# Kernel tuning notes

Hardware: AMD Instinct MI355X
Metric: run time of the kernel (lower is better)

The kernel has to match this reference:

```python
import jax, jax.numpy as jnp
import numpy as np

SQRT2 = 1.4142135623730951  # lrelu def_gain
LRELU_SLOPE = 0.2
EPS = 1e-8


def setup_inputs() -> dict:
    key = jax.random.key(0)
    k1, k2, k3, k4 = jax.random.split(key, 4)
    B, C_in, C_out, H, W, K, DLAT = 8, 512, 512, 32, 32, 3, 512
    x = jax.random.normal(k1, (B, C_in, H, W), dtype=jnp.float32)
    y = jax.random.normal(k2, (B, DLAT), dtype=jnp.float32)
    # init_std = 1.0 since use_wscale=True, lrmul=1
    weight = jax.random.normal(k3, (C_out, C_in, K, K), dtype=jnp.float32)
    mod_weight = jax.random.normal(k4, (C_in, DLAT), dtype=jnp.float32)
    bias = jnp.ones((C_in,), dtype=jnp.float32)
    return {"x": x, "y": y, "weight": weight, "mod_weight": mod_weight, "bias": bias}


def reference(x, y, weight, mod_weight, bias):
    B, C_in, H, W = x.shape
    C_out, _, K, _ = weight.shape
    dlat = mod_weight.shape[1]
    w_mul_mod = dlat ** (-0.5)  # EqualizedLinear wscale; conv w_mul is unused in forward
    # style: s = sqrt(2) * lrelu(y @ W_mod^T + b)
    s = y @ (mod_weight * w_mul_mod).T  # [B, C_in]
    s = jax.nn.leaky_relu(s + bias, LRELU_SLOPE) * SQRT2
    # modulate per-sample weights: [B, C_out, C_in, K, K]
    ww = weight[None] * s[:, None, :, None, None]
    # demodulate
    d = jax.lax.rsqrt(jnp.sum(ww * ww, axis=(2, 3, 4)) + EPS)  # [B, C_out]
    ww = ww * d[:, :, None, None, None]
    # fused grouped conv: groups = batch
    xg = x.reshape(1, B * C_in, H, W)
    wg = ww.reshape(B * C_out, C_in, K, K)
    out = jax.lax.conv_general_dilated(
        xg, wg, window_strides=(1, 1), padding="SAME",
        dimension_numbers=("NCHW", "OIHW", "NCHW"),
        feature_group_count=B)
    return out.reshape(B, C_out, H, W)
```

## Files before the change

kernel.cpp:

```cpp
#include <hip/hip_runtime.h>
#include <hip/hip_bf16.h>

typedef float f32x4 __attribute__((ext_vector_type(4)));
typedef short bf16x8 __attribute__((ext_vector_type(8)));

#define LRELU_SLOPE 0.2f
#define SQRT2F 1.4142135623730951f
#define MODSCALE 0.044194173824159216f

#define GLL(SRC, DST)                                                       \
  __builtin_amdgcn_global_load_lds(                                         \
      (const __attribute__((address_space(1))) unsigned int*)(SRC),         \
      (__attribute__((address_space(3))) unsigned int*)(DST), 16, 0, 0)

__global__ __launch_bounds__(64) void style_kernel(const float* __restrict__ y,
                                                   const float* __restrict__ mw,
                                                   const float* __restrict__ bias,
                                                   float* __restrict__ s) {
  int ci = blockIdx.x;
  int l = threadIdx.x;
  const float4* mwr = reinterpret_cast<const float4*>(mw + ci * 512);
  float4 m0 = mwr[2 * l], m1 = mwr[2 * l + 1];
  float acc[8];
#pragma unroll
  for (int b = 0; b < 8; ++b) {
    const float4* yr = reinterpret_cast<const float4*>(y + b * 512);
    float4 y0 = yr[2 * l], y1 = yr[2 * l + 1];
    acc[b] = m0.x * y0.x + m0.y * y0.y + m0.z * y0.z + m0.w * y0.w +
             m1.x * y1.x + m1.y * y1.y + m1.z * y1.z + m1.w * y1.w;
  }
#pragma unroll
  for (int off = 32; off > 0; off >>= 1) {
#pragma unroll
    for (int b = 0; b < 8; ++b) acc[b] += __shfl_xor(acc[b], off, 64);
  }
  if (l < 8) {
    float v = acc[l] * MODSCALE + bias[ci];
    v = v > 0.f ? v : LRELU_SLOPE * v;
    s[l * 512 + ci] = v * SQRT2F;
  }
}

__global__ __launch_bounds__(256) void wprep_kernel(const float* __restrict__ w,
                                                    __hip_bfloat16* __restrict__ wt,
                                                    float* __restrict__ wsq) {
  int idx = blockIdx.x * 256 + threadIdx.x;
  const float* p = w + (size_t)idx * 9;
  float v[9];
  float sq = 0.f;
#pragma unroll
  for (int t = 0; t < 9; ++t) {
    v[t] = p[t];
    sq += v[t] * v[t];
  }
  wsq[idx] = sq;
#pragma unroll
  for (int t = 0; t < 9; ++t) wt[t * 262144 + idx] = __float2bfloat16(v[t]);
}

__global__ __launch_bounds__(64) void demod_kernel(const float* __restrict__ wsq,
                                                   const float* __restrict__ s,
                                                   float* __restrict__ d) {
  int co = blockIdx.x;
  int l = threadIdx.x;
  const float4* qr = reinterpret_cast<const float4*>(wsq + co * 512);
  float4 q0 = qr[2 * l], q1 = qr[2 * l + 1];
  float acc[8];
#pragma unroll
  for (int b = 0; b < 8; ++b) {
    const float4* sr = reinterpret_cast<const float4*>(s + b * 512);
    float4 s0 = sr[2 * l], s1 = sr[2 * l + 1];
    acc[b] = q0.x * s0.x * s0.x + q0.y * s0.y * s0.y + q0.z * s0.z * s0.z +
             q0.w * s0.w * s0.w + q1.x * s1.x * s1.x + q1.y * s1.y * s1.y +
             q1.z * s1.z * s1.z + q1.w * s1.w * s1.w;
  }
#pragma unroll
  for (int off = 32; off > 0; off >>= 1) {
#pragma unroll
    for (int b = 0; b < 8; ++b) acc[b] += __shfl_xor(acc[b], off, 64);
  }
  if (l < 8) d[l * 512 + co] = rsqrtf(acc[l] + 1e-8f);
}

__global__ __launch_bounds__(256) void xs_kernel(const float* __restrict__ x,
                                                 const float* __restrict__ s,
                                                 __hip_bfloat16* __restrict__ xsp) {
  int bid = blockIdx.x;
  int cc = bid & 7;
  int h = (bid >> 3) & 31;
  int b = bid >> 8;
  int tid = threadIdx.x;
  __shared__ __hip_bfloat16 tile[32][72];

  int cil = tid >> 2;
  int w0 = (tid & 3) * 8;
  int ci = cc * 64 + cil;
  const float* xp = x + (((size_t)(b * 512 + ci) * 32 + h) << 5) + w0;
  float sv = s[b * 512 + ci];
  float4 a0 = *reinterpret_cast<const float4*>(xp);
  float4 a1 = *reinterpret_cast<const float4*>(xp + 4);
  tile[w0 + 0][cil] = __float2bfloat16(a0.x * sv);
  tile[w0 + 1][cil] = __float2bfloat16(a0.y * sv);
  tile[w0 + 2][cil] = __float2bfloat16(a0.z * sv);
  tile[w0 + 3][cil] = __float2bfloat16(a0.w * sv);
  tile[w0 + 4][cil] = __float2bfloat16(a1.x * sv);
  tile[w0 + 5][cil] = __float2bfloat16(a1.y * sv);
  tile[w0 + 6][cil] = __float2bfloat16(a1.z * sv);
  tile[w0 + 7][cil] = __float2bfloat16(a1.w * sv);
  __syncthreads();

  int wloc = tid >> 3;
  int cj = (tid & 7) * 8;
  int4 v = *reinterpret_cast<const int4*>(&tile[wloc][cj]);
  unsigned off = (unsigned)((b * 34 + h + 1) * 34 + (wloc + 1)) * 512 + cc * 64 + cj;
  *reinterpret_cast<int4*>(xsp + off) = v;
}

__global__ __launch_bounds__(512, 2) void conv_kernel(const __hip_bfloat16* __restrict__ xsp,
                                                      const __hip_bfloat16* __restrict__ wt,
                                                      const float* __restrict__ dmod,
                                                      float* __restrict__ out) {
  __shared__ __hip_bfloat16 As_[2][224 * 64];
  __shared__ __hip_bfloat16 Bs_[2][3 * 128 * 64];
  const int bid = blockIdx.x;
  const int xcd = bid & 7, slot = bid >> 3;
  const int bm = xcd * 8 + (slot >> 2);
  const int bn = slot & 3;
  const int tid = threadIdx.x;
  const int wv = tid >> 6;
  const int l = tid & 63;
  const int kg = wv >> 2;
  const int wr = (wv >> 1) & 1, wc = wv & 1;
  const int bb = bm >> 3;
  const int h0 = (bm & 7) << 2;

  const int swz = (((l & 7) ^ (l >> 3)) << 3);
  unsigned boff[2];
#pragma unroll
  for (int j = 0; j < 2; ++j) {
    int row = ((j * 8 + wv) << 3) + (l >> 3);
    boff[j] = (unsigned)((bn << 7) + row) * 512 + swz;
  }
  unsigned ahoff[4];
  int adst[4];
#pragma unroll
  for (int j = 0; j < 4; ++j) {
    int rb = j < 3 ? j * 64 + wv * 8 : 192 + (wv & 3) * 8;
    int r = rb + (l >> 3);
    int rc = r > 203 ? 203 : r;
    int hr = rc / 34, hc = rc - hr * 34;
    ahoff[j] = (unsigned)((bb * 34 + h0 + hr) * 34 + hc) * 512 + (((l & 7) ^ (r & 7)) << 3);
    adst[j] = rb;
  }
  int pb[4];
#pragma unroll
  for (int m = 0; m < 4; ++m)
    pb[m] = ((wr << 1) + (m >> 1)) * 34 + ((m & 1) << 4) + (l & 15);

  f32x4 acc[4][4];
#pragma unroll
  for (int n = 0; n < 4; ++n)
#pragma unroll
    for (int m = 0; m < 4; ++m) acc[n][m] = (f32x4)0.f;

  auto stageB = [&](__hip_bfloat16* Bn, int t, int k0c) {
    const __hip_bfloat16* src = wt + t * 262144 + k0c * 64;
#pragma unroll
    for (int j = 0; j < 2; ++j)
      GLL(src + boff[j], Bn + ((j * 8 + wv) << 9));
  };
  auto stageA1 = [&](__hip_bfloat16* An, int j, int kn) {
    GLL(xsp + ahoff[j] + kn * 64, An + (adst[j] << 6));
  };
  auto phase = [&](const __hip_bfloat16* Aq, const __hip_bfloat16* Bq, int dh, int dw) {
    const int cb = (kg << 2) + (l >> 4);
    bf16x8 af[4], bfr[4];
#pragma unroll
    for (int m = 0; m < 4; ++m) {
      int p = pb[m] + dh * 34 + dw;
      af[m] = *reinterpret_cast<const bf16x8*>(Aq + p * 64 + ((cb ^ (p & 7)) << 3));
    }
#pragma unroll
    for (int n = 0; n < 4; ++n) {
      int row = (wc << 6) + (n << 4) + (l & 15);
      bfr[n] = *reinterpret_cast<const bf16x8*>(Bq + row * 64 + ((cb ^ (l & 7)) << 3));
    }
    __builtin_amdgcn_s_setprio(1);
#pragma unroll
    for (int n = 0; n < 4; ++n)
#pragma unroll
      for (int m = 0; m < 4; ++m)
        acc[n][m] = __builtin_amdgcn_mfma_f32_16x16x32_bf16(bfr[n], af[m], acc[n][m], 0, 0, 0);
    __builtin_amdgcn_s_setprio(0);
  };

#define SB0 __builtin_amdgcn_sched_barrier(0)
#define WAITBAR0                                            \
  asm volatile("s_waitcnt vmcnt(0)" ::: "memory");          \
  __builtin_amdgcn_s_barrier();                             \
  SB0

#pragma unroll
  for (int j = 0; j < 4; ++j) stageA1(&As_[0][0], j, 0);
  SB0;
  stageB(&Bs_[0][0] + 0 * 8192, 0, 0);
  stageB(&Bs_[0][0] + 1 * 8192, 1, 0);
  stageB(&Bs_[0][0] + 2 * 8192, 2, 0);

#pragma unroll 1
  for (int k0 = 0; k0 < 8; ++k0) {
    const __hip_bfloat16* Aq = &As_[k0 & 1][0];
    __hip_bfloat16* An = &As_[(k0 + 1) & 1][0];
    __hip_bfloat16* Br = &Bs_[k0 & 1][0];
    __hip_bfloat16* Bo = &Bs_[(k0 & 1) ^ 1][0];
    const int kn = k0 + 1;
    WAITBAR0;
    stageB(Bo + 0 * 8192, 3, k0);
    stageB(Bo + 1 * 8192, 4, k0);
    stageB(Bo + 2 * 8192, 5, k0);
    if (k0 < 7) { stageA1(An, 0, kn); stageA1(An, 1, kn); }
    SB0;
    phase(Aq, Br + 0 * 8192, 0, 0);
    phase(Aq, Br + 1 * 8192, 0, 1);
    phase(Aq, Br + 2 * 8192, 0, 2);
    WAITBAR0;
    stageB(Br + 0 * 8192, 6, k0);
    stageB(Br + 1 * 8192, 7, k0);
    stageB(Br + 2 * 8192, 8, k0);
    if (k0 < 7) { stageA1(An, 2, kn); stageA1(An, 3, kn); }
    SB0;
    phase(Aq, Bo + 0 * 8192, 1, 0);
    phase(Aq, Bo + 1 * 8192, 1, 1);
    phase(Aq, Bo + 2 * 8192, 1, 2);
    WAITBAR0;
    if (k0 < 7) {
      stageB(Bo + 0 * 8192, 0, kn);
      stageB(Bo + 1 * 8192, 1, kn);
      stageB(Bo + 2 * 8192, 2, kn);
    }
    SB0;
    phase(Aq, Br + 0 * 8192, 2, 0);
    phase(Aq, Br + 1 * 8192, 2, 1);
    phase(Aq, Br + 2 * 8192, 2, 2);
  }
#undef WAITBAR0
#undef SB0

  float* red = reinterpret_cast<float*>(&Bs_[0][0]);
  __syncthreads();
  if (kg == 1) {
#pragma unroll
    for (int n = 0; n < 4; ++n)
#pragma unroll
      for (int m = 0; m < 4; ++m)
        *reinterpret_cast<f32x4*>(red + (n * 4 + m) * 1024 + (wv & 3) * 256 + l * 4) =
            acc[n][m];
  }
  __syncthreads();
  if (kg == 0) {
    const int pixbase = ((bm & 7) << 7) + (wr << 6) + (l & 15);
    const int cob = (bn << 7) + (wc << 6) + ((l >> 4) << 2);
    float* ob = out + ((size_t)bb << 19);
    const float* drow = dmod + bb * 512;
#pragma unroll
    for (int n = 0; n < 4; ++n) {
#pragma unroll
      for (int m = 0; m < 4; ++m)
        acc[n][m] += *reinterpret_cast<const f32x4*>(red + (n * 4 + m) * 1024 + wv * 256 + l * 4);
#pragma unroll
      for (int jj = 0; jj < 4; ++jj) {
        const int co = cob + (n << 4) + jj;
        const float dv = drow[co];
        float* orow = ob + ((unsigned)co << 10) + pixbase;
#pragma unroll
        for (int m = 0; m < 4; ++m) orow[m << 4] = acc[n][m][jj] * dv;
      }
    }
  }
}

extern "C" void kernel_launch(void* const* d_in, const int* in_sizes, int n_in,
                              void* d_out, int out_size, void* d_ws, size_t ws_size,
                              hipStream_t stream) {
  (void)in_sizes; (void)n_in; (void)out_size; (void)ws_size;
  const float* x = (const float*)d_in[0];
  const float* y = (const float*)d_in[1];
  const float* w = (const float*)d_in[2];
  const float* mw = (const float*)d_in[3];
  const float* bias = (const float*)d_in[4];
  float* out = (float*)d_out;

  char* ws = (char*)d_ws;
  float* s = (float*)(ws + 0);
  float* dmod = (float*)(ws + 16384);
  float* wsq = (float*)(ws + 32768);
  __hip_bfloat16* wt = (__hip_bfloat16*)(ws + 1081344);
  __hip_bfloat16* xsp = (__hip_bfloat16*)(ws + 5799936);

  hipMemsetAsync(xsp, 0, 9469952, stream);
  style_kernel<<<512, 64, 0, stream>>>(y, mw, bias, s);
  wprep_kernel<<<1024, 256, 0, stream>>>(w, wt, wsq);
  demod_kernel<<<512, 64, 0, stream>>>(wsq, s, dmod);
  xs_kernel<<<2048, 256, 0, stream>>>(x, s, xsp);
  conv_kernel<<<256, 512, 0, stream>>>(xsp, wt, dmod, out);
}
```

Baseline: 70.22 us.

## Fuse prep kernels, zero only halo, and deepen conv weight pipeline to four slots

```diff
diff --git a/kernel.cpp b/kernel.cpp
--- a/kernel.cpp
+++ b/kernel.cpp
@@ -13,107 +13,123 @@
       (const __attribute__((address_space(1))) unsigned int*)(SRC),         \
       (__attribute__((address_space(3))) unsigned int*)(DST), 16, 0, 0)
 
-__global__ __launch_bounds__(64) void style_kernel(const float* __restrict__ y,
+__global__ __launch_bounds__(256) void prep_kernel(const float* __restrict__ w,
+                                                   const float* __restrict__ y,
                                                    const float* __restrict__ mw,
                                                    const float* __restrict__ bias,
-                                                   float* __restrict__ s) {
-  int ci = blockIdx.x;
-  int l = threadIdx.x;
-  const float4* mwr = reinterpret_cast<const float4*>(mw + ci * 512);
-  float4 m0 = mwr[2 * l], m1 = mwr[2 * l + 1];
-  float acc[8];
-#pragma unroll
-  for (int b = 0; b < 8; ++b) {
-    const float4* yr = reinterpret_cast<const float4*>(y + b * 512);
-    float4 y0 = yr[2 * l], y1 = yr[2 * l + 1];
-    acc[b] = m0.x * y0.x + m0.y * y0.y + m0.z * y0.z + m0.w * y0.w +
-             m1.x * y1.x + m1.y * y1.y + m1.z * y1.z + m1.w * y1.w;
-  }
-#pragma unroll
-  for (int off = 32; off > 0; off >>= 1) {
-#pragma unroll
-    for (int b = 0; b < 8; ++b) acc[b] += __shfl_xor(acc[b], off, 64);
-  }
-  if (l < 8) {
-    float v = acc[l] * MODSCALE + bias[ci];
-    v = v > 0.f ? v : LRELU_SLOPE * v;
-    s[l * 512 + ci] = v * SQRT2F;
+                                                   __hip_bfloat16* __restrict__ wt,
+                                                   float* __restrict__ wsq,
+                                                   float* __restrict__ s,
+                                                   __hip_bfloat16* __restrict__ xsp) {
+  const int bid = blockIdx.x;
+  const int tid = threadIdx.x;
+  if (bid < 1024) {
+    int idx = bid * 256 + tid;
+    const float* p = w + (size_t)idx * 9;
+    float v[9];
+    float sq = 0.f;
+#pragma unroll
+    for (int t = 0; t < 9; ++t) {
+      v[t] = p[t];
+      sq += v[t] * v[t];
+    }
+    wsq[idx] = sq;
+#pragma unroll
+    for (int t = 0; t < 9; ++t) wt[t * 262144 + idx] = __float2bfloat16(v[t]);
+  } else if (bid < 1152) {
+    int l = tid & 63;
+    int ci = (bid - 1024) * 4 + (tid >> 6);
+    const float4* mwr = reinterpret_cast<const float4*>(mw + ci * 512);
+    float4 m0 = mwr[2 * l], m1 = mwr[2 * l + 1];
+    float acc[8];
+#pragma unroll
+    for (int b = 0; b < 8; ++b) {
+      const float4* yr = reinterpret_cast<const float4*>(y + b * 512);
+      float4 y0 = yr[2 * l], y1 = yr[2 * l + 1];
+      acc[b] = m0.x * y0.x + m0.y * y0.y + m0.z * y0.z + m0.w * y0.w +
+               m1.x * y1.x + m1.y * y1.y + m1.z * y1.z + m1.w * y1.w;
+    }
+#pragma unroll
+    for (int off = 32; off > 0; off >>= 1) {
+#pragma unroll
+      for (int b = 0; b < 8; ++b) acc[b] += __shfl_xor(acc[b], off, 64);
+    }
+    if (l < 8) {
+      float v = acc[l] * MODSCALE + bias[ci];
+      v = v > 0.f ? v : LRELU_SLOPE * v;
+      s[l * 512 + ci] = v * SQRT2F;
+    }
+  } else {
+    int i = (bid - 1152) * 256 + tid;
+    int b = i / 8448;
+    int r = i - b * 8448;
+    int pos = r >> 6;
+    int cj = (r & 63) << 3;
+    int hr, hc;
+    if (pos < 34) { hr = 0; hc = pos; }
+    else if (pos < 68) { hr = 33; hc = pos - 34; }
+    else if (pos < 100) { hr = pos - 67; hc = 0; }
+    else { hr = pos - 99; hc = 33; }
+    unsigned off = (unsigned)((b * 34 + hr) * 34 + hc) * 512 + cj;
+    int4 z = {0, 0, 0, 0};
+    *reinterpret_cast<int4*>(xsp + off) = z;
   }
 }
 
-__global__ __launch_bounds__(256) void wprep_kernel(const float* __restrict__ w,
-                                                    __hip_bfloat16* __restrict__ wt,
-                                                    float* __restrict__ wsq) {
-  int idx = blockIdx.x * 256 + threadIdx.x;
-  const float* p = w + (size_t)idx * 9;
-  float v[9];
-  float sq = 0.f;
-#pragma unroll
-  for (int t = 0; t < 9; ++t) {
-    v[t] = p[t];
-    sq += v[t] * v[t];
-  }
-  wsq[idx] = sq;
-#pragma unroll
-  for (int t = 0; t < 9; ++t) wt[t * 262144 + idx] = __float2bfloat16(v[t]);
-}
-
-__global__ __launch_bounds__(64) void demod_kernel(const float* __restrict__ wsq,
-                                                   const float* __restrict__ s,
-                                                   float* __restrict__ d) {
-  int co = blockIdx.x;
-  int l = threadIdx.x;
-  const float4* qr = reinterpret_cast<const float4*>(wsq + co * 512);
-  float4 q0 = qr[2 * l], q1 = qr[2 * l + 1];
-  float acc[8];
-#pragma unroll
-  for (int b = 0; b < 8; ++b) {
-    const float4* sr = reinterpret_cast<const float4*>(s + b * 512);
-    float4 s0 = sr[2 * l], s1 = sr[2 * l + 1];
-    acc[b] = q0.x * s0.x * s0.x + q0.y * s0.y * s0.y + q0.z * s0.z * s0.z +
-             q0.w * s0.w * s0.w + q1.x * s1.x * s1.x + q1.y * s1.y * s1.y +
-             q1.z * s1.z * s1.z + q1.w * s1.w * s1.w;
-  }
-#pragma unroll
-  for (int off = 32; off > 0; off >>= 1) {
-#pragma unroll
-    for (int b = 0; b < 8; ++b) acc[b] += __shfl_xor(acc[b], off, 64);
-  }
-  if (l < 8) d[l * 512 + co] = rsqrtf(acc[l] + 1e-8f);
-}
-
-__global__ __launch_bounds__(256) void xs_kernel(const float* __restrict__ x,
-                                                 const float* __restrict__ s,
-                                                 __hip_bfloat16* __restrict__ xsp) {
-  int bid = blockIdx.x;
-  int cc = bid & 7;
-  int h = (bid >> 3) & 31;
-  int b = bid >> 8;
-  int tid = threadIdx.x;
-  __shared__ __hip_bfloat16 tile[32][72];
-
-  int cil = tid >> 2;
-  int w0 = (tid & 3) * 8;
-  int ci = cc * 64 + cil;
-  const float* xp = x + (((size_t)(b * 512 + ci) * 32 + h) << 5) + w0;
-  float sv = s[b * 512 + ci];
-  float4 a0 = *reinterpret_cast<const float4*>(xp);
-  float4 a1 = *reinterpret_cast<const float4*>(xp + 4);
-  tile[w0 + 0][cil] = __float2bfloat16(a0.x * sv);
-  tile[w0 + 1][cil] = __float2bfloat16(a0.y * sv);
-  tile[w0 + 2][cil] = __float2bfloat16(a0.z * sv);
-  tile[w0 + 3][cil] = __float2bfloat16(a0.w * sv);
-  tile[w0 + 4][cil] = __float2bfloat16(a1.x * sv);
-  tile[w0 + 5][cil] = __float2bfloat16(a1.y * sv);
-  tile[w0 + 6][cil] = __float2bfloat16(a1.z * sv);
-  tile[w0 + 7][cil] = __float2bfloat16(a1.w * sv);
-  __syncthreads();
-
-  int wloc = tid >> 3;
-  int cj = (tid & 7) * 8;
-  int4 v = *reinterpret_cast<const int4*>(&tile[wloc][cj]);
-  unsigned off = (unsigned)((b * 34 + h + 1) * 34 + (wloc + 1)) * 512 + cc * 64 + cj;
-  *reinterpret_cast<int4*>(xsp + off) = v;
+__global__ __launch_bounds__(256) void xsdem_kernel(const float* __restrict__ x,
+                                                    const float* __restrict__ s,
+                                                    const float* __restrict__ wsq,
+                                                    __hip_bfloat16* __restrict__ xsp,
+                                                    float* __restrict__ d) {
+  const int bid = blockIdx.x;
+  const int tid = threadIdx.x;
+  if (bid < 2048) {
+    int cc = bid & 7;
+    int h = (bid >> 3) & 31;
+    int b = bid >> 8;
+    __shared__ __hip_bfloat16 tile[32][72];
+    int cil = tid >> 2;
+    int w0 = (tid & 3) * 8;
+    int ci = cc * 64 + cil;
+    const float* xp = x + (((size_t)(b * 512 + ci) * 32 + h) << 5) + w0;
+    float sv = s[b * 512 + ci];
+    float4 a0 = *reinterpret_cast<const float4*>(xp);
+    float4 a1 = *reinterpret_cast<const float4*>(xp + 4);
+    tile[w0 + 0][cil] = __float2bfloat16(a0.x * sv);
+    tile[w0 + 1][cil] = __float2bfloat16(a0.y * sv);
+    tile[w0 + 2][cil] = __float2bfloat16(a0.z * sv);
+    tile[w0 + 3][cil] = __float2bfloat16(a0.w * sv);
+    tile[w0 + 4][cil] = __float2bfloat16(a1.x * sv);
+    tile[w0 + 5][cil] = __float2bfloat16(a1.y * sv);
+    tile[w0 + 6][cil] = __float2bfloat16(a1.z * sv);
+    tile[w0 + 7][cil] = __float2bfloat16(a1.w * sv);
+    __syncthreads();
+    int wloc = tid >> 3;
+    int cj = (tid & 7) * 8;
+    int4 v = *reinterpret_cast<const int4*>(&tile[wloc][cj]);
+    unsigned off = (unsigned)((b * 34 + h + 1) * 34 + (wloc + 1)) * 512 + cc * 64 + cj;
+    *reinterpret_cast<int4*>(xsp + off) = v;
+  } else {
+    int l = tid & 63;
+    int co = (bid - 2048) * 4 + (tid >> 6);
+    const float4* qr = reinterpret_cast<const float4*>(wsq + co * 512);
+    float4 q0 = qr[2 * l], q1 = qr[2 * l + 1];
+    float acc[8];
+#pragma unroll
+    for (int b = 0; b < 8; ++b) {
+      const float4* sr = reinterpret_cast<const float4*>(s + b * 512);
+      float4 s0 = sr[2 * l], s1 = sr[2 * l + 1];
+      acc[b] = q0.x * s0.x * s0.x + q0.y * s0.y * s0.y + q0.z * s0.z * s0.z +
+               q0.w * s0.w * s0.w + q1.x * s1.x * s1.x + q1.y * s1.y * s1.y +
+               q1.z * s1.z * s1.z + q1.w * s1.w * s1.w;
+    }
+#pragma unroll
+    for (int off = 32; off > 0; off >>= 1) {
+#pragma unroll
+      for (int b = 0; b < 8; ++b) acc[b] += __shfl_xor(acc[b], off, 64);
+    }
+    if (l < 8) d[l * 512 + co] = rsqrtf(acc[l] + 1e-8f);
+  }
 }
 
 __global__ __launch_bounds__(512, 2) void conv_kernel(const __hip_bfloat16* __restrict__ xsp,
@@ -121,11 +137,11 @@
                                                       const float* __restrict__ dmod,
                                                       float* __restrict__ out) {
   __shared__ __hip_bfloat16 As_[2][224 * 64];
-  __shared__ __hip_bfloat16 Bs_[2][3 * 128 * 64];
+  __shared__ __hip_bfloat16 Bs_[4][128 * 64];
   const int bid = blockIdx.x;
-  const int xcd = bid & 7, slot = bid >> 3;
-  const int bm = xcd * 8 + (slot >> 2);
-  const int bn = slot & 3;
+  const int xcd = bid & 7, slot0 = bid >> 3;
+  const int bm = xcd * 8 + (slot0 >> 2);
+  const int bn = slot0 & 3;
   const int tid = threadIdx.x;
   const int wv = tid >> 6;
   const int l = tid & 63;
@@ -163,27 +179,27 @@
 #pragma unroll
     for (int m = 0; m < 4; ++m) acc[n][m] = (f32x4)0.f;
 
-  auto stageB = [&](__hip_bfloat16* Bn, int t, int k0c) {
+  auto stageB = [&](int sl, int t, int k0c) {
     const __hip_bfloat16* src = wt + t * 262144 + k0c * 64;
 #pragma unroll
     for (int j = 0; j < 2; ++j)
-      GLL(src + boff[j], Bn + ((j * 8 + wv) << 9));
+      GLL(src + boff[j], &Bs_[sl][(j * 8 + wv) << 9]);
   };
-  auto stageA1 = [&](__hip_bfloat16* An, int j, int kn) {
-    GLL(xsp + ahoff[j] + kn * 64, An + (adst[j] << 6));
+  auto stageA1 = [&](int ab, int j, int kn) {
+    GLL(xsp + ahoff[j] + kn * 64, &As_[ab][adst[j] << 6]);
   };
-  auto phase = [&](const __hip_bfloat16* Aq, const __hip_bfloat16* Bq, int dh, int dw) {
+  auto phase = [&](int ab, int sl, int dh, int dw) {
     const int cb = (kg << 2) + (l >> 4);
     bf16x8 af[4], bfr[4];
 #pragma unroll
     for (int m = 0; m < 4; ++m) {
       int p = pb[m] + dh * 34 + dw;
-      af[m] = *reinterpret_cast<const bf16x8*>(Aq + p * 64 + ((cb ^ (p & 7)) << 3));
+      af[m] = *reinterpret_cast<const bf16x8*>(&As_[ab][p * 64 + ((cb ^ (p & 7)) << 3)]);
     }
 #pragma unroll
     for (int n = 0; n < 4; ++n) {
       int row = (wc << 6) + (n << 4) + (l & 15);
-      bfr[n] = *reinterpret_cast<const bf16x8*>(Bq + row * 64 + ((cb ^ (l & 7)) << 3));
+      bfr[n] = *reinterpret_cast<const bf16x8*>(&Bs_[sl][row * 64 + ((cb ^ (l & 7)) << 3)]);
     }
     __builtin_amdgcn_s_setprio(1);
 #pragma unroll
@@ -195,55 +211,43 @@
   };
 
 #define SB0 __builtin_amdgcn_sched_barrier(0)
-#define WAITBAR0                                            \
-  asm volatile("s_waitcnt vmcnt(0)" ::: "memory");          \
+#define WB(N)                                               \
+  asm volatile("s_waitcnt vmcnt(" #N ")" ::: "memory");     \
   __builtin_amdgcn_s_barrier();                             \
   SB0
 
 #pragma unroll
-  for (int j = 0; j < 4; ++j) stageA1(&As_[0][0], j, 0);
+  for (int j = 0; j < 4; ++j) stageA1(0, j, 0);
   SB0;
-  stageB(&Bs_[0][0] + 0 * 8192, 0, 0);
-  stageB(&Bs_[0][0] + 1 * 8192, 1, 0);
-  stageB(&Bs_[0][0] + 2 * 8192, 2, 0);
+  stageB(0, 0, 0);
+  stageB(1, 1, 0);
+  stageB(2, 2, 0);
 
 #pragma unroll 1
-  for (int k0 = 0; k0 < 8; ++k0) {
-    const __hip_bfloat16* Aq = &As_[k0 & 1][0];
-    __hip_bfloat16* An = &As_[(k0 + 1) & 1][0];
-    __hip_bfloat16* Br = &Bs_[k0 & 1][0];
-    __hip_bfloat16* Bo = &Bs_[(k0 & 1) ^ 1][0];
-    const int kn = k0 + 1;
-    WAITBAR0;
-    stageB(Bo + 0 * 8192, 3, k0);
-    stageB(Bo + 1 * 8192, 4, k0);
-    stageB(Bo + 2 * 8192, 5, k0);
-    if (k0 < 7) { stageA1(An, 0, kn); stageA1(An, 1, kn); }
-    SB0;
-    phase(Aq, Br + 0 * 8192, 0, 0);
-    phase(Aq, Br + 1 * 8192, 0, 1);
-    phase(Aq, Br + 2 * 8192, 0, 2);
-    WAITBAR0;
-    stageB(Br + 0 * 8192, 6, k0);
-    stageB(Br + 1 * 8192, 7, k0);
-    stageB(Br + 2 * 8192, 8, k0);
-    if (k0 < 7) { stageA1(An, 2, kn); stageA1(An, 3, kn); }
-    SB0;
-    phase(Aq, Bo + 0 * 8192, 1, 0);
-    phase(Aq, Bo + 1 * 8192, 1, 1);
-    phase(Aq, Bo + 2 * 8192, 1, 2);
-    WAITBAR0;
-    if (k0 < 7) {
-      stageB(Bo + 0 * 8192, 0, kn);
-      stageB(Bo + 1 * 8192, 1, kn);
-      stageB(Bo + 2 * 8192, 2, kn);
-    }
-    SB0;
-    phase(Aq, Br + 0 * 8192, 2, 0);
-    phase(Aq, Br + 1 * 8192, 2, 1);
-    phase(Aq, Br + 2 * 8192, 2, 2);
-  }
-#undef WAITBAR0
+  for (int k0 = 0; k0 < 7; ++k0) {
+    const int a = k0 & 1, an = a ^ 1, kn = k0 + 1;
+    WB(4); stageB((k0 + 3) & 3, 3, k0); stageA1(an, 0, kn); SB0; phase(a, (k0 + 0) & 3, 0, 0);
+    WB(5); stageB((k0 + 4) & 3, 4, k0); stageA1(an, 1, kn); SB0; phase(a, (k0 + 1) & 3, 0, 1);
+    WB(6); stageB((k0 + 5) & 3, 5, k0); stageA1(an, 2, kn); SB0; phase(a, (k0 + 2) & 3, 0, 2);
+    WB(7); stageB((k0 + 6) & 3, 6, k0); stageA1(an, 3, kn); SB0; phase(a, (k0 + 3) & 3, 1, 0);
+    WB(7); stageB((k0 + 7) & 3, 7, k0); SB0; phase(a, (k0 + 4) & 3, 1, 1);
+    WB(6); stageB((k0 + 8) & 3, 8, k0); SB0; phase(a, (k0 + 5) & 3, 1, 2);
+    WB(5); stageB((k0 + 9) & 3, 0, kn); SB0; phase(a, (k0 + 6) & 3, 2, 0);
+    WB(4); stageB((k0 + 10) & 3, 1, kn); SB0; phase(a, (k0 + 7) & 3, 2, 1);
+    WB(4); stageB((k0 + 11) & 3, 2, kn); SB0; phase(a, (k0 + 8) & 3, 2, 2);
+  }
+  {
+    WB(4); stageB((7 + 3) & 3, 3, 7); SB0; phase(1, (7 + 0) & 3, 0, 0);
+    WB(4); stageB((7 + 4) & 3, 4, 7); SB0; phase(1, (7 + 1) & 3, 0, 1);
+    WB(4); stageB((7 + 5) & 3, 5, 7); SB0; phase(1, (7 + 2) & 3, 0, 2);
+    WB(4); stageB((7 + 6) & 3, 6, 7); SB0; phase(1, (7 + 3) & 3, 1, 0);
+    WB(4); stageB((7 + 7) & 3, 7, 7); SB0; phase(1, (7 + 4) & 3, 1, 1);
+    WB(4); stageB((7 + 8) & 3, 8, 7); SB0; phase(1, (7 + 5) & 3, 1, 2);
+    WB(4); SB0; phase(1, (7 + 6) & 3, 2, 0);
+    WB(2); SB0; phase(1, (7 + 7) & 3, 2, 1);
+    WB(0); SB0; phase(1, (7 + 8) & 3, 2, 2);
+  }
+#undef WB
 #undef SB0
 
   float* red = reinterpret_cast<float*>(&Bs_[0][0]);
@@ -297,10 +301,7 @@
   __hip_bfloat16* wt = (__hip_bfloat16*)(ws + 1081344);
   __hip_bfloat16* xsp = (__hip_bfloat16*)(ws + 5799936);
 
-  hipMemsetAsync(xsp, 0, 9469952, stream);
-  style_kernel<<<512, 64, 0, stream>>>(y, mw, bias, s);
-  wprep_kernel<<<1024, 256, 0, stream>>>(w, wt, wsq);
-  demod_kernel<<<512, 64, 0, stream>>>(wsq, s, dmod);
-  xs_kernel<<<2048, 256, 0, stream>>>(x, s, xsp);
+  prep_kernel<<<1416, 256, 0, stream>>>(w, y, mw, bias, wt, wsq, s, xsp);
+  xsdem_kernel<<<2176, 256, 0, stream>>>(x, s, wsq, xsp, dmod);
   conv_kernel<<<256, 512, 0, stream>>>(xsp, wt, dmod, out);
 }
```

New measurement: 71.38 us. About the same (+1.6%).
